# Optimization experiments

Measured on AMD Instinct MI355X. Metric: run time of the kernel, lower is better.

The kernel has to match this reference:

```python
import jax, jax.numpy as jnp
import numpy as np

LAMBDA_ENTROPY = 0.1
LAMBDA_REPULSION = 0.5
LAMBDA_INTER = 0.3
TEMPERATURE = 1.0
EPS = 1e-8


def setup_inputs() -> dict:
    key = jax.random.key(0)
    k1, k2 = jax.random.split(key)
    membership = jax.random.uniform(k1, (16384, 64, 32), dtype=jnp.float32)   # (N,F,K) soft bin assignments
    teacher_preds = jax.random.uniform(k2, (16384, 128), dtype=jnp.float32)   # (N,C)
    return {"membership": membership, "teacher_preds": teacher_preds}


def reference(membership, teacher_preds):
    N, F, K = membership.shape
    # --- weighted centroids per (feature, bin) ---
    bin_mass = membership.sum(axis=0) + EPS                       # (F,K)
    sum_weighted_y = jnp.einsum('nfk,nc->fkc', membership, teacher_preds)  # avoids (N,F,K,C)
    centroids = sum_weighted_y / bin_mass[..., None]              # (F,K,C)
    # --- weighted intra-bin variance: ||y_n - c_fk||^2 expanded, no (N,F,K,C) tensor ---
    y_sq = jnp.sum(teacher_preds * teacher_preds, axis=-1)        # (N,)
    c_sq = jnp.sum(centroids * centroids, axis=-1)                # (F,K)
    cross = jnp.einsum('nc,fkc->nfk', teacher_preds, centroids)   # (N,F,K)
    dist_sq = y_sq[:, None, None] + c_sq[None, :, :] - 2.0 * cross
    weighted_variance = jnp.sum(membership * dist_sq, axis=0) / bin_mass  # (F,K)
    loss_dispersion = weighted_variance.sum()
    # --- bin-occupancy entropy ---
    p_bins = bin_mass / N                                         # (F,K)
    loss_entropy = jnp.sum(p_bins * jnp.log(p_bins + EPS))
    # --- neighbor repulsion between adjacent bin centroids ---
    neighbor_dist = jnp.sum((centroids[:, :-1, :] - centroids[:, 1:, :]) ** 2, axis=-1)  # (F,K-1)
    loss_repulsion = jnp.sum(jnp.exp(-neighbor_dist / TEMPERATURE))
    # --- all-pairs inter-bin dispersion, batched over F (replaces python loop) ---
    dots = jnp.einsum('fkc,fjc->fkj', centroids, centroids)       # (F,K,K)
    pairwise = c_sq[:, :, None] + c_sq[:, None, :] - 2.0 * dots
    triu = jnp.triu(jnp.ones((K, K), dtype=centroids.dtype), k=1)  # strictly upper
    loss_inter = jnp.sum(jnp.exp(-pairwise / TEMPERATURE) * triu) / F
    total = (loss_dispersion
             + LAMBDA_ENTROPY * loss_entropy
             + LAMBDA_REPULSION * loss_repulsion
             + LAMBDA_INTER * loss_inter)
    return total, loss_dispersion, loss_entropy, loss_repulsion, loss_inter
```

## Files before the change

### kernel.cpp

```cpp
#include <hip/hip_runtime.h>
#include <math.h>

#define N_PTS   16384
#define F_DIM   64
#define K_BINS  32
#define C_DIM   128
#define FK      2048
#define CP      144
#define CW      132
#define EPS_F   1e-8f

typedef _Float16 f16x8 __attribute__((ext_vector_type(8)));
typedef float    f32x4 __attribute__((ext_vector_type(4)));

static __device__ inline unsigned pack_h2(float a, float b) {
    union { _Float16 h[2]; unsigned u; } x;
    x.h[0] = (_Float16)a; x.h[1] = (_Float16)b;
    return x.u;
}

__global__ __launch_bounds__(256) void build_yt_k(const float* __restrict__ Y,
                                                  _Float16* __restrict__ Yt) {
    __shared__ __align__(16) float Yl[64][132];
    __shared__ float ysql[64];
    const int t  = threadIdx.x;
    const int n0 = blockIdx.x * 64;
    const int nl = t >> 5;
    const int c4 = t & 31;
#pragma unroll
    for (int p = 0; p < 8; ++p) {
        const int n = p * 8 + nl;
        const float4 v = reinterpret_cast<const float4*>(Y + (size_t)(n0 + n) * C_DIM)[c4];
        reinterpret_cast<float4*>(Yl[n])[c4] = v;
        float sq = v.x * v.x + v.y * v.y + v.z * v.z + v.w * v.w;
#pragma unroll
        for (int m = 16; m >= 1; m >>= 1) sq += __shfl_xor(sq, m, 64);
        if (c4 == 0) ysql[n] = sq;
    }
    __syncthreads();
    unsigned* YtU = (unsigned*)Yt;
    const int nd0 = n0 >> 1;
    const int n2  = t & 31;
    const int rr  = t >> 5;
#pragma unroll
    for (int p = 0; p < 16; ++p) {
        const int c = p * 8 + rr;
        YtU[(size_t)c * (N_PTS / 2) + nd0 + n2] = pack_h2(Yl[2 * n2][c], Yl[2 * n2 + 1][c]);
    }
    if (t < 32) {
        YtU[(size_t)128 * (N_PTS / 2) + nd0 + t] = pack_h2(ysql[2 * t], ysql[2 * t + 1]);
    } else if (t < 64) {
        YtU[(size_t)129 * (N_PTS / 2) + nd0 + (t - 32)] = 0x3C003C00u;
    }
    for (int idx = t; idx < 14 * 32; idx += 256) {
        YtU[(size_t)(130 + (idx >> 5)) * (N_PTS / 2) + nd0 + (idx & 31)] = 0u;
    }
}

__global__ __launch_bounds__(256) void gemm_k(const float* __restrict__ M,
                                              const _Float16* __restrict__ Yt,
                                              float* __restrict__ wpart,
                                              int cn) {
    const int t    = threadIdx.x;
    const int fk0  = blockIdx.x * 64;
    const int ch   = blockIdx.y;
    const int n0   = ch * cn;
    const int w    = t >> 6;
    const int l    = t & 63;
    const int quad = l >> 4;
    const int cl   = l & 15;
    const int fkA  = fk0 + w * 16 + cl;
    const _Float16* yt = Yt + (size_t)cl * N_PTS;
    const float*    mp = M + fkA;

    f32x4 acc[9] = {};
    f16x8 b0[9], b1[9];
    float a0r[8], a1r[8];

    int nbase = n0 + quad * 8;
#pragma unroll
    for (int ct = 0; ct < 9; ++ct)
        b0[ct] = *reinterpret_cast<const f16x8*>(yt + (size_t)(ct * 16) * N_PTS + nbase);
#pragma unroll
    for (int j = 0; j < 8; ++j)
        a0r[j] = mp[(size_t)(nbase + j) * FK];

    for (int nb = 0; nb < cn; nb += 64) {
        const int nb1 = nbase + 32;
#pragma unroll
        for (int ct = 0; ct < 9; ++ct)
            b1[ct] = *reinterpret_cast<const f16x8*>(yt + (size_t)(ct * 16) * N_PTS + nb1);
#pragma unroll
        for (int j = 0; j < 8; ++j)
            a1r[j] = mp[(size_t)(nb1 + j) * FK];
        {
            f16x8 a;
#pragma unroll
            for (int j = 0; j < 8; ++j) a[j] = (_Float16)a0r[j];
#pragma unroll
            for (int ct = 0; ct < 9; ++ct)
                acc[ct] = __builtin_amdgcn_mfma_f32_16x16x32_f16(a, b0[ct], acc[ct], 0, 0, 0);
        }
        const int nb2 = nbase + 64;
        if (nb + 64 < cn) {
#pragma unroll
            for (int ct = 0; ct < 9; ++ct)
                b0[ct] = *reinterpret_cast<const f16x8*>(yt + (size_t)(ct * 16) * N_PTS + nb2);
#pragma unroll
            for (int j = 0; j < 8; ++j)
                a0r[j] = mp[(size_t)(nb2 + j) * FK];
        }
        {
            f16x8 a;
#pragma unroll
            for (int j = 0; j < 8; ++j) a[j] = (_Float16)a1r[j];
#pragma unroll
            for (int ct = 0; ct < 9; ++ct)
                acc[ct] = __builtin_amdgcn_mfma_f32_16x16x32_f16(a, b1[ct], acc[ct], 0, 0, 0);
        }
        nbase = nb2;
    }

    float* wp = wpart + (size_t)ch * FK * CW;
#pragma unroll
    for (int ct = 0; ct < 9; ++ct) {
        const int c = ct * 16 + cl;
        if (c < CW) {
#pragma unroll
            for (int r = 0; r < 4; ++r) {
                const int fk = fk0 + w * 16 + quad * 4 + r;
                wp[(size_t)fk * CW + c] = acc[ct][r];
            }
        }
    }
}

__global__ __launch_bounds__(128) void reduce_w_k(const float* __restrict__ wpart,
                                                  float* __restrict__ W, int nchunk) {
    const int idx = blockIdx.x * 128 + threadIdx.x;
    const float4* src = reinterpret_cast<const float4*>(wpart);
    const size_t cs = (size_t)FK * CW / 4;
    float4 s0 = make_float4(0.f, 0.f, 0.f, 0.f), s1 = s0, s2 = s0, s3 = s0;
    int ch = 0;
    for (; ch + 3 < nchunk; ch += 4) {
        const float4 a = src[idx + (size_t)(ch + 0) * cs];
        const float4 b = src[idx + (size_t)(ch + 1) * cs];
        const float4 c = src[idx + (size_t)(ch + 2) * cs];
        const float4 d = src[idx + (size_t)(ch + 3) * cs];
        s0.x += a.x; s0.y += a.y; s0.z += a.z; s0.w += a.w;
        s1.x += b.x; s1.y += b.y; s1.z += b.z; s1.w += b.w;
        s2.x += c.x; s2.y += c.y; s2.z += c.z; s2.w += c.w;
        s3.x += d.x; s3.y += d.y; s3.z += d.z; s3.w += d.w;
    }
    for (; ch < nchunk; ++ch) {
        const float4 a = src[idx + (size_t)ch * cs];
        s0.x += a.x; s0.y += a.y; s0.z += a.z; s0.w += a.w;
    }
    float4 r;
    r.x = (s0.x + s1.x) + (s2.x + s3.x);
    r.y = (s0.y + s1.y) + (s2.y + s3.y);
    r.z = (s0.z + s1.z) + (s2.z + s3.z);
    r.w = (s0.w + s1.w) + (s2.w + s3.w);
    reinterpret_cast<float4*>(W)[idx] = r;
}

__global__ __launch_bounds__(256) void epilogue_k(const float* __restrict__ W,
                                                  float* __restrict__ fpart) {
    __shared__ __align__(16) float Wl[32][CW];
    __shared__ float Bv[32], Binv[32], S1v[32], csq[32];
    __shared__ float scr[32][8];
    __shared__ float4 red4[256];
    const int t = threadIdx.x;
    const int f = blockIdx.x;

    for (int e = t; e < 32 * 33; e += 256) {
        const int k = e / 33, c4 = e % 33;
        reinterpret_cast<float4*>(Wl[k])[c4] =
            reinterpret_cast<const float4*>(W + (size_t)(f * 32 + k) * CW)[c4];
    }
    __syncthreads();
    if (t < 32) {
        const float B = Wl[t][129] + EPS_F;
        Bv[t] = B; Binv[t] = 1.0f / B; S1v[t] = Wl[t][128];
    }
    __syncthreads();
    {
        const int k = t >> 3, g = t & 7;
        const float ib = Binv[k];
        float s = 0.f;
        for (int c = g * 16; c < g * 16 + 16; ++c) {
            const float v = Wl[k][c] * ib;
            Wl[k][c] = v;
            s = fmaf(v, v, s);
        }
        scr[k][g] = s;
    }
    __syncthreads();
    if (t < 32) {
        float s = 0.f;
#pragma unroll
        for (int g = 0; g < 8; ++g) s += scr[t][g];
        csq[t] = s;
    }
    __syncthreads();

    float my_disp = 0.f, my_ent = 0.f, my_rep = 0.f, my_inter = 0.f;
    if (t < 32) {
        my_disp = (S1v[t] - csq[t] * (Bv[t] + EPS_F)) * Binv[t];
        const float p = Bv[t] * (1.0f / (float)N_PTS);
        my_ent = p * logf(p + EPS_F);
    }
    {
        const int pr = t >> 3, g = t & 7;
        float s = 0.f;
        if (pr < 31) {
            for (int c = g * 16; c < g * 16 + 16; ++c) {
                const float d = Wl[pr][c] - Wl[pr + 1][c];
                s = fmaf(d, d, s);
            }
        }
        __syncthreads();
        scr[pr][g] = s;
    }
    __syncthreads();
    if (t < 31) {
        float d = 0.f;
#pragma unroll
        for (int g = 0; g < 8; ++g) d += scr[t][g];
        my_rep = expf(-d);
    }
#pragma unroll
    for (int s4 = 0; s4 < 4; ++s4) {
        const int slot = t + s4 * 256;
        const int k = slot >> 5, j = slot & 31;
        if (k < j) {
            float dot = 0.f;
            for (int c4 = 0; c4 < 32; ++c4) {
                const float4 a = reinterpret_cast<const float4*>(Wl[k])[c4];
                const float4 b = reinterpret_cast<const float4*>(Wl[j])[c4];
                dot = fmaf(a.x, b.x, dot); dot = fmaf(a.y, b.y, dot);
                dot = fmaf(a.z, b.z, dot); dot = fmaf(a.w, b.w, dot);
            }
            my_inter += expf(-(csq[k] + csq[j] - 2.0f * dot));
        }
    }
    red4[t] = make_float4(my_disp, my_ent, my_rep, my_inter);
    __syncthreads();
    for (int off = 128; off >= 1; off >>= 1) {
        if (t < off) {
            const float4 a = red4[t], b = red4[t + off];
            red4[t] = make_float4(a.x + b.x, a.y + b.y, a.z + b.z, a.w + b.w);
        }
        __syncthreads();
    }
    if (t == 0) {
        fpart[f * 4 + 0] = red4[0].x;
        fpart[f * 4 + 1] = red4[0].y;
        fpart[f * 4 + 2] = red4[0].z;
        fpart[f * 4 + 3] = red4[0].w;
    }
}

__global__ void final_reduce_k(const float* __restrict__ fpart,
                               float* __restrict__ out) {
    const int t = threadIdx.x;
    float4 v = reinterpret_cast<const float4*>(fpart)[t];
#pragma unroll
    for (int m = 32; m >= 1; m >>= 1) {
        v.x += __shfl_xor(v.x, m, 64);
        v.y += __shfl_xor(v.y, m, 64);
        v.z += __shfl_xor(v.z, m, 64);
        v.w += __shfl_xor(v.w, m, 64);
    }
    if (t == 0) {
        const float disp  = v.x, ent = v.y, rep = v.z;
        const float inter = v.w * (1.0f / (float)F_DIM);
        out[0] = disp + 0.1f * ent + 0.5f * rep + 0.3f * inter;
        out[1] = disp;
        out[2] = ent;
        out[3] = rep;
        out[4] = inter;
    }
}

extern "C" void kernel_launch(void* const* d_in, const int* in_sizes, int n_in,
                              void* d_out, int out_size, void* d_ws, size_t ws_size,
                              hipStream_t stream) {
    const float* M = (const float*)d_in[0];
    const float* Y = (const float*)d_in[1];
    float* out = (float*)d_out;
    char*  ws  = (char*)d_ws;

    const size_t ytBytes = (size_t)CP * N_PTS * sizeof(_Float16);
    const size_t wBytes  = (size_t)FK * CW * sizeof(float);

    _Float16* Yt    = (_Float16*)ws;
    float*    W     = (float*)(ws + ytBytes);
    float*    fpart = (float*)(ws + ytBytes + wBytes);
    float*    wpart = (float*)(ws + ytBytes + wBytes + 1024);

    const size_t used = ytBytes + wBytes + 1024;
    int nchunk = 32;
    while (nchunk > 1 && used + (size_t)nchunk * wBytes > ws_size) nchunk >>= 1;
    const int cn = N_PTS / nchunk;

    build_yt_k<<<dim3(N_PTS / 64), dim3(256), 0, stream>>>(Y, Yt);
    gemm_k<<<dim3(32, nchunk), dim3(256), 0, stream>>>(M, Yt, wpart, cn);
    reduce_w_k<<<dim3(FK * CW / 4 / 128), dim3(128), 0, stream>>>(wpart, W, nchunk);
    epilogue_k<<<dim3(F_DIM), dim3(256), 0, stream>>>(W, fpart);
    final_reduce_k<<<dim3(1), dim3(64), 0, stream>>>(fpart, out);
}
```

Baseline: 270.0 us.

## Pre-swizzle Y into MFMA fragment layout and stage B via LDS async loads

The Y preprocessing now writes a fp16 buffer already in per-lane MFMA B-fragment order, with 9 column tiles per 32-row block, replacing the transposed row-major layout. The GEMM kernel loads B fragments cooperatively into double-buffered shared memory using global_load_lds, so the 4 waves share one copy instead of each wave loading all 9 tiles itself. This cuts redundant global B traffic and register pressure, at the cost of extra __syncthreads per step and an LDS round trip.

```diff
diff --git a/kernel.cpp b/kernel.cpp
--- a/kernel.cpp
+++ b/kernel.cpp
@@ -6,21 +6,15 @@
 #define K_BINS  32
 #define C_DIM   128
 #define FK      2048
-#define CP      144
+#define NB32    (N_PTS / 32)
 #define CW      132
 #define EPS_F   1e-8f
 
 typedef _Float16 f16x8 __attribute__((ext_vector_type(8)));
 typedef float    f32x4 __attribute__((ext_vector_type(4)));
 
-static __device__ inline unsigned pack_h2(float a, float b) {
-    union { _Float16 h[2]; unsigned u; } x;
-    x.h[0] = (_Float16)a; x.h[1] = (_Float16)b;
-    return x.u;
-}
-
-__global__ __launch_bounds__(256) void build_yt_k(const float* __restrict__ Y,
-                                                  _Float16* __restrict__ Yt) {
+__global__ __launch_bounds__(256) void build_ybf_k(const float* __restrict__ Y,
+                                                   _Float16* __restrict__ Ybf) {
     __shared__ __align__(16) float Yl[64][132];
     __shared__ float ysql[64];
     const int t  = threadIdx.x;
@@ -38,88 +32,113 @@
         if (c4 == 0) ysql[n] = sq;
     }
     __syncthreads();
-    unsigned* YtU = (unsigned*)Yt;
-    const int nd0 = n0 >> 1;
-    const int n2  = t & 31;
-    const int rr  = t >> 5;
-#pragma unroll
-    for (int p = 0; p < 16; ++p) {
-        const int c = p * 8 + rr;
-        YtU[(size_t)c * (N_PTS / 2) + nd0 + n2] = pack_h2(Yl[2 * n2][c], Yl[2 * n2 + 1][c]);
-    }
-    if (t < 32) {
-        YtU[(size_t)128 * (N_PTS / 2) + nd0 + t] = pack_h2(ysql[2 * t], ysql[2 * t + 1]);
-    } else if (t < 64) {
-        YtU[(size_t)129 * (N_PTS / 2) + nd0 + (t - 32)] = 0x3C003C00u;
-    }
-    for (int idx = t; idx < 14 * 32; idx += 256) {
-        YtU[(size_t)(130 + (idx >> 5)) * (N_PTS / 2) + nd0 + (idx & 31)] = 0u;
+    for (int p = 0; p < 5; ++p) {
+        const int s = t + p * 256;
+        if (s < 1152) {
+            const int nb2  = s / 576;
+            const int r    = s % 576;
+            const int ct   = r >> 6;
+            const int l    = r & 63;
+            const int quad = l >> 4, cl = l & 15;
+            const int nloc = nb2 * 32 + quad * 8;
+            f16x8 v;
+            if (ct < 8) {
+                const int c = ct * 16 + cl;
+#pragma unroll
+                for (int j = 0; j < 8; ++j) v[j] = (_Float16)Yl[nloc + j][c];
+            } else if (cl == 0) {
+#pragma unroll
+                for (int j = 0; j < 8; ++j) v[j] = (_Float16)ysql[nloc + j];
+            } else if (cl == 1) {
+#pragma unroll
+                for (int j = 0; j < 8; ++j) v[j] = (_Float16)1.0f;
+            } else {
+#pragma unroll
+                for (int j = 0; j < 8; ++j) v[j] = (_Float16)0.0f;
+            }
+            const int nb = blockIdx.x * 2 + nb2;
+            *reinterpret_cast<f16x8*>(Ybf + ((size_t)(ct * NB32 + nb) * 64 + l) * 8) = v;
+        }
     }
 }
 
 __global__ __launch_bounds__(256) void gemm_k(const float* __restrict__ M,
-                                              const _Float16* __restrict__ Yt,
+                                              const _Float16* __restrict__ Ybf,
                                               float* __restrict__ wpart,
                                               int cn) {
+    __shared__ __align__(16) _Float16 Bb[2][9][512];
     const int t    = threadIdx.x;
     const int fk0  = blockIdx.x * 64;
     const int ch   = blockIdx.y;
     const int n0   = ch * cn;
+    const int nb0  = n0 >> 5;
     const int w    = t >> 6;
     const int l    = t & 63;
     const int quad = l >> 4;
     const int cl   = l & 15;
     const int fkA  = fk0 + w * 16 + cl;
-    const _Float16* yt = Yt + (size_t)cl * N_PTS;
-    const float*    mp = M + fkA;
+    const float* mp = M + fkA;
+    const int steps = cn >> 5;
 
     f32x4 acc[9] = {};
-    f16x8 b0[9], b1[9];
     float a0r[8], a1r[8];
 
-    int nbase = n0 + quad * 8;
-#pragma unroll
-    for (int ct = 0; ct < 9; ++ct)
-        b0[ct] = *reinterpret_cast<const f16x8*>(yt + (size_t)(ct * 16) * N_PTS + nbase);
-#pragma unroll
-    for (int j = 0; j < 8; ++j)
-        a0r[j] = mp[(size_t)(nbase + j) * FK];
-
-    for (int nb = 0; nb < cn; nb += 64) {
-        const int nb1 = nbase + 32;
-#pragma unroll
-        for (int ct = 0; ct < 9; ++ct)
-            b1[ct] = *reinterpret_cast<const f16x8*>(yt + (size_t)(ct * 16) * N_PTS + nb1);
-#pragma unroll
-        for (int j = 0; j < 8; ++j)
-            a1r[j] = mp[(size_t)(nb1 + j) * FK];
+#define STAGE(s, par)                                                          \
+    {                                                                          \
+        const int nb_ = nb0 + (s);                                             \
+        _Pragma("unroll")                                                      \
+        for (int ct = w; ct < 9; ct += 4) {                                    \
+            const _Float16* g_ = Ybf + ((size_t)(ct * NB32 + nb_) * 64 + l) * 8; \
+            __builtin_amdgcn_global_load_lds(                                  \
+                (const __attribute__((address_space(1))) unsigned*)g_,         \
+                (__attribute__((address_space(3))) unsigned*)&Bb[par][ct][0],  \
+                16, 0, 0);                                                     \
+        }                                                                      \
+    }
+#define LOADA(ar, s)                                                           \
+    {                                                                          \
+        const size_t nbase_ = (size_t)(n0 + (s) * 32 + quad * 8);              \
+        _Pragma("unroll")                                                      \
+        for (int j = 0; j < 8; ++j) ar[j] = mp[(nbase_ + j) * FK];             \
+    }
+
+    STAGE(0, 0); LOADA(a0r, 0);
+    STAGE(1, 1); LOADA(a1r, 1);
+
+    for (int s = 0; s < steps; s += 2) {
+        __syncthreads();
         {
-            f16x8 a;
-#pragma unroll
-            for (int j = 0; j < 8; ++j) a[j] = (_Float16)a0r[j];
+            f16x8 bf[9];
 #pragma unroll
             for (int ct = 0; ct < 9; ++ct)
-                acc[ct] = __builtin_amdgcn_mfma_f32_16x16x32_f16(a, b0[ct], acc[ct], 0, 0, 0);
-        }
-        const int nb2 = nbase + 64;
-        if (nb + 64 < cn) {
+                bf[ct] = *reinterpret_cast<const f16x8*>(&Bb[0][ct][l * 8]);
+            f16x8 af;
+#pragma unroll
+            for (int j = 0; j < 8; ++j) af[j] = (_Float16)a0r[j];
+            __syncthreads();
+            if (s + 2 < steps) { STAGE(s + 2, 0); LOADA(a0r, s + 2); }
 #pragma unroll
             for (int ct = 0; ct < 9; ++ct)
-                b0[ct] = *reinterpret_cast<const f16x8*>(yt + (size_t)(ct * 16) * N_PTS + nb2);
-#pragma unroll
-            for (int j = 0; j < 8; ++j)
-                a0r[j] = mp[(size_t)(nb2 + j) * FK];
-        }
+                acc[ct] = __builtin_amdgcn_mfma_f32_16x16x32_f16(af, bf[ct], acc[ct], 0, 0, 0);
+        }
+        __syncthreads();
         {
-            f16x8 a;
-#pragma unroll
-            for (int j = 0; j < 8; ++j) a[j] = (_Float16)a1r[j];
+            f16x8 bf[9];
 #pragma unroll
             for (int ct = 0; ct < 9; ++ct)
-                acc[ct] = __builtin_amdgcn_mfma_f32_16x16x32_f16(a, b1[ct], acc[ct], 0, 0, 0);
-        }
-        nbase = nb2;
-    }
+                bf[ct] = *reinterpret_cast<const f16x8*>(&Bb[1][ct][l * 8]);
+            f16x8 af;
+#pragma unroll
+            for (int j = 0; j < 8; ++j) af[j] = (_Float16)a1r[j];
+            __syncthreads();
+            if (s + 3 < steps) { STAGE(s + 3, 1); LOADA(a1r, s + 3); }
+#pragma unroll
+            for (int ct = 0; ct < 9; ++ct)
+                acc[ct] = __builtin_amdgcn_mfma_f32_16x16x32_f16(af, bf[ct], acc[ct], 0, 0, 0);
+        }
+    }
+#undef STAGE
+#undef LOADA
 
     float* wp = wpart + (size_t)ch * FK * CW;
 #pragma unroll
@@ -291,21 +310,21 @@
     float* out = (float*)d_out;
     char*  ws  = (char*)d_ws;
 
-    const size_t ytBytes = (size_t)CP * N_PTS * sizeof(_Float16);
-    const size_t wBytes  = (size_t)FK * CW * sizeof(float);
-
-    _Float16* Yt    = (_Float16*)ws;
-    float*    W     = (float*)(ws + ytBytes);
-    float*    fpart = (float*)(ws + ytBytes + wBytes);
-    float*    wpart = (float*)(ws + ytBytes + wBytes + 1024);
-
-    const size_t used = ytBytes + wBytes + 1024;
+    const size_t ybfBytes = (size_t)9 * NB32 * 64 * 8 * sizeof(_Float16);
+    const size_t wBytes   = (size_t)FK * CW * sizeof(float);
+
+    _Float16* Ybf   = (_Float16*)ws;
+    float*    W     = (float*)(ws + ybfBytes);
+    float*    fpart = (float*)(ws + ybfBytes + wBytes);
+    float*    wpart = (float*)(ws + ybfBytes + wBytes + 1024);
+
+    const size_t used = ybfBytes + wBytes + 1024;
     int nchunk = 32;
     while (nchunk > 1 && used + (size_t)nchunk * wBytes > ws_size) nchunk >>= 1;
     const int cn = N_PTS / nchunk;
 
-    build_yt_k<<<dim3(N_PTS / 64), dim3(256), 0, stream>>>(Y, Yt);
-    gemm_k<<<dim3(32, nchunk), dim3(256), 0, stream>>>(M, Yt, wpart, cn);
+    build_ybf_k<<<dim3(N_PTS / 64), dim3(256), 0, stream>>>(Y, Ybf);
+    gemm_k<<<dim3(32, nchunk), dim3(256), 0, stream>>>(M, Ybf, wpart, cn);
     reduce_w_k<<<dim3(FK * CW / 4 / 128), dim3(128), 0, stream>>>(wpart, W, nchunk);
     epilogue_k<<<dim3(F_DIM), dim3(256), 0, stream>>>(W, fpart);
     final_reduce_k<<<dim3(1), dim3(64), 0, stream>>>(fpart, out);
```

After: 233.6 us. -13.5%, faster.
